# Kernel tuning notes

Hardware: AMD Instinct MI355X
Metric: run time of the kernel (lower is better)

Reference implementation:

```python
import jax, jax.numpy as jnp
import numpy as np

B, S, D, H, E, KW = 2, 2048, 1024, 8, 128, 16  # batch, seq, d_model, heads, head_width, kernel_width


def setup_inputs() -> dict:
    key = jax.random.key(0)
    ks = jax.random.split(key, 10)
    sc = D ** -0.5
    x = jax.random.normal(ks[0], (B, S, D), dtype=jnp.float32)
    Wq = jax.random.normal(ks[1], (H, D, E), dtype=jnp.float32) * sc
    bq = jnp.zeros((H, E), dtype=jnp.float32)
    Wk = jax.random.normal(ks[2], (H, D, E), dtype=jnp.float32) * sc
    bk = jnp.zeros((H, E), dtype=jnp.float32)
    Wv = jax.random.normal(ks[3], (H, D, E), dtype=jnp.float32) * sc
    bv = jnp.zeros((H, E), dtype=jnp.float32)
    Wo = jax.random.normal(ks[4], (H, E, D), dtype=jnp.float32) * ((H * E) ** -0.5)
    bo = jnp.zeros((D,), dtype=jnp.float32)
    dilations = jnp.array([1, 1, 2, 2, 4, 4, 8, 8], dtype=jnp.int32)
    return {"x": x, "Wq": Wq, "bq": bq, "Wk": Wk, "bk": bk,
            "Wv": Wv, "bv": bv, "Wo": Wo, "bo": bo, "dilations": dilations}


def _windows(kh, vh, bkh, bvh, d):
    # kh, vh: [B, S, E] projected keys/values for one head; d: dilation (scalar int)
    s = kh.shape[1]
    # center-justified dilated window: positions i + d*j - d*(KW-1)//2
    pos = jnp.arange(s)[:, None] + d * jnp.arange(KW)[None, :] - (d * (KW - 1)) // 2
    valid = (pos >= 0) & (pos < s)            # [S, KW]
    posc = jnp.clip(pos, 0, s - 1)
    # padded positions hold the zero-embedding, whose projection is just the bias
    kw = jnp.where(valid[None, :, :, None], kh[:, posc, :], bkh)  # [B, S, KW, E]
    vw = jnp.where(valid[None, :, :, None], vh[:, posc, :], bvh)
    return kw, vw


def _lcsa(x, Wq, bq, Wk, bk, Wv, bv, Wo, bo, dilations):
    # per-head independent projections (Core.Linear with parallel shape [heads])
    q = jnp.einsum('bsd,hde->bhse', x, Wq) + bq[None, :, None, :]       # [B,H,S,E]
    k_all = jnp.einsum('bsd,hde->bhse', x, Wk) + bk[None, :, None, :]
    v_all = jnp.einsum('bsd,hde->bhse', x, Wv) + bv[None, :, None, :]
    # gather dilated local windows per head (project-then-gather; padded = bias)
    kw, vw = jax.vmap(_windows, in_axes=(1, 1, 0, 0, 0))(k_all, v_all, bk, bv, dilations)
    # kw, vw: [H, B, S, KW, E]
    logits = jnp.einsum('bhse,hbske->bhsk', q, kw)                       # [B,H,S,KW]
    score = jax.nn.softmax(logits, axis=-1)
    # NOTE: original divides by sqrt(d_head) AFTER softmax*value (faithful quirk)
    attn = jnp.einsum('bhsk,hbske->bhse', score, vw) / jnp.sqrt(jnp.asarray(E, x.dtype))
    out = jnp.einsum('bhse,hed->bsd', attn, Wo) + bo                     # dehead merge
    return out


def reference(x, Wq, bq, Wk, bk, Wv, bv, Wo, bo, dilations):
    return _lcsa(x, Wq, bq, Wk, bk, Wv, bv, Wo, bo, dilations)
```

## Files before the change

kernel.cpp:

```cpp
#include <hip/hip_runtime.h>
#include <stdint.h>

#define Bb 2
#define Ss 2048
#define Dd 1024
#define Hh 8
#define Ee 128
#define KWW 16
#define Mm (Bb*Ss)
#define Kk 1024

typedef unsigned short u16;
typedef __attribute__((ext_vector_type(8))) _Float16 f16x8;
typedef __attribute__((ext_vector_type(4))) float f32x4;

__device__ __forceinline__ u16 f2h(float f) {
  union { _Float16 h; u16 u; } v; v.h = (_Float16)f; return v.u;
}
__device__ __forceinline__ float h2f(u16 u) {
  union { u16 u; _Float16 h; } v; v.u = u; return (float)v.h;
}
__device__ __forceinline__ float h2f_lo(uint32_t w) { return h2f((u16)(w & 0xFFFF)); }
__device__ __forceinline__ float h2f_hi(uint32_t w) { return h2f((u16)(w >> 16)); }

__device__ __forceinline__ void gll16(const void* g, void* l) {
  __builtin_amdgcn_global_load_lds((const __attribute__((address_space(1))) void*)g,
                                   (__attribute__((address_space(3))) void*)l, 16, 0, 0);
}


__global__ __launch_bounds__(256) void cast_f32_f16(const float* __restrict__ in,
                                                    u16* __restrict__ out, int n) {
  int i = (blockIdx.x * 256 + threadIdx.x) * 4;
  if (i < n) {
    float4 f = *(const float4*)(in + i);
    uint64_t pk = (uint64_t)f2h(f.x) | ((uint64_t)f2h(f.y) << 16) |
                  ((uint64_t)f2h(f.z) << 32) | ((uint64_t)f2h(f.w) << 48);
    *(uint64_t*)(out + i) = pk;
  }
}

__global__ __launch_bounds__(256) void transpose_qkv(
    const float* __restrict__ Wq, const float* __restrict__ Wk,
    const float* __restrict__ Wv, u16* __restrict__ wT) {
  __shared__ float tile[32][33];
  const int z = blockIdx.z, h = z & 7;
  const float* W = (z < 8) ? Wq : (z < 16) ? Wk : Wv;
  const float* ib = W + (size_t)h * Dd * Ee;
  u16* ob = wT + (size_t)z * Ee * Kk;
  int r0 = blockIdx.x * 32, c0 = blockIdx.y * 32;
  int tx = threadIdx.x, ty = threadIdx.y;
  #pragma unroll
  for (int kq = 0; kq < 4; kq++)
    tile[ty + 8*kq][tx] = ib[(size_t)(r0 + ty + 8*kq) * Ee + (c0 + tx)];
  __syncthreads();
  #pragma unroll
  for (int kq = 0; kq < 4; kq++)
    ob[(size_t)(c0 + ty + 8*kq) * Dd + (r0 + tx)] = f2h(tile[tx][ty + 8*kq]);
}

__global__ __launch_bounds__(256) void transpose_wo(
    const float* __restrict__ in, u16* __restrict__ out) {
  __shared__ float tile[32][33];
  const int R = Hh * Ee, C = Dd;
  int r0 = blockIdx.x * 32, c0 = blockIdx.y * 32;
  int tx = threadIdx.x, ty = threadIdx.y;
  #pragma unroll
  for (int kq = 0; kq < 4; kq++)
    tile[ty + 8*kq][tx] = in[(size_t)(r0 + ty + 8*kq) * C + (c0 + tx)];
  __syncthreads();
  #pragma unroll
  for (int kq = 0; kq < 4; kq++)
    out[(size_t)(c0 + ty + 8*kq) * R + (r0 + tx)] = f2h(tile[tx][ty + 8*kq]);
}

template<int MT>
__device__ __forceinline__ void gemm_core(
    const u16* __restrict__ A, const u16* __restrict__ Bt,
    u16* As, u16* Bs, f32x4 (&acc)[MT / 32][4]) {
  constexpr int MI = MT / 32;
  const int tid = threadIdx.x;
  const int wave = tid >> 6;
  const int lane = tid & 63;
  const int srow = wave * 16 + (lane >> 2);
  const int skc  = (lane & 3) * 8;
  const size_t go0 = (size_t)srow        * Kk + skc;
  const size_t go1 = (size_t)(srow + 64) * Kk + skc;
  u16* al0 = As + wave * 512;
  u16* al1 = As + 2048 + wave * 512;
  u16* bl0 = Bs + wave * 512;
  u16* bl1 = Bs + 2048 + wave * 512;

  const int wm = (wave >> 1) * (MT / 2);
  const int wn = (wave & 1) * 64;
  const int fr = lane & 15;
  const int fk = (lane >> 4) * 8;

  #pragma unroll
  for (int i = 0; i < MI; i++)
    #pragma unroll
    for (int j = 0; j < 4; j++)
      #pragma unroll
      for (int r = 0; r < 4; r++) acc[i][j][r] = 0.0f;

  for (int kt = 0; kt < Kk; kt += 32) {
    gll16(A + go0 + kt, al0);
    if constexpr (MT == 128) gll16(A + go1 + kt, al1);
    gll16(Bt + go0 + kt, bl0);
    gll16(Bt + go1 + kt, bl1);
    __syncthreads();
    f16x8 ah[MI], bh[4];
    #pragma unroll
    for (int i = 0; i < MI; i++)
      ah[i] = *(const f16x8*)(As + (wm + i * 16 + fr) * 32 + fk);
    #pragma unroll
    for (int j = 0; j < 4; j++)
      bh[j] = *(const f16x8*)(Bs + (wn + j * 16 + fr) * 32 + fk);
    #pragma unroll
    for (int i = 0; i < MI; i++)
      #pragma unroll
      for (int j = 0; j < 4; j++)
        acc[i][j] = __builtin_amdgcn_mfma_f32_16x16x32_f16(ah[i], bh[j], acc[i][j], 0, 0, 0);
    __syncthreads();
  }
}


__global__ __launch_bounds__(256) void gemm_qkv(
    const u16* __restrict__ xh, const u16* __restrict__ wT,
    const float* __restrict__ bq, const float* __restrict__ bk, const float* __restrict__ bv,
    u16* __restrict__ q, u16* __restrict__ k, u16* __restrict__ v) {
  __shared__ u16 As[128 * 32];
  __shared__ u16 Bs[128 * 32];
  const int m0 = blockIdx.x * 128;
  const int z = blockIdx.z;
  const int proj = z >> 3, h = z & 7;
  f32x4 acc[4][4];
  gemm_core<128>(xh + (size_t)m0 * Kk, wT + (size_t)z * (Ee * Kk), As, Bs, acc);

  u16* dst = proj == 0 ? q : (proj == 1 ? k : v);
  const float* bias = proj == 0 ? bq : (proj == 1 ? bk : bv);
  const int wave = threadIdx.x >> 6, lane = threadIdx.x & 63;
  const int wm = (wave >> 1) * 64, wn = (wave & 1) * 64;
  const int cn = lane & 15, rq4 = (lane >> 4) * 4;
  #pragma unroll
  for (int j = 0; j < 4; j++) {
    const int e = wn + j * 16 + cn;
    const float bb = bias[h * Ee + e];
    #pragma unroll
    for (int i = 0; i < 4; i++) {
      #pragma unroll
      for (int r = 0; r < 4; r++) {
        const int m = m0 + wm + i * 16 + rq4 + r;
        const int b = m >> 11, s = m & (Ss - 1);
        dst[(((size_t)(b * Hh + h)) * Ss + s) * Ee + e] = f2h(acc[i][j][r] + bb);
      }
    }
  }
}

__global__ __launch_bounds__(256) void gemm_out(
    const u16* __restrict__ attn, const u16* __restrict__ woT,
    const float* __restrict__ bo, float* __restrict__ out) {
  __shared__ u16 As[64 * 32];
  __shared__ u16 Bs[128 * 32];
  const int m0 = blockIdx.x * 64;
  const int n0 = blockIdx.y * 128;
  f32x4 acc[2][4];
  gemm_core<64>(attn + (size_t)m0 * Kk, woT + (size_t)n0 * Kk, As, Bs, acc);
  const int wave = threadIdx.x >> 6, lane = threadIdx.x & 63;
  const int wm = (wave >> 1) * 32, wn = (wave & 1) * 64;
  const int cn = lane & 15, rq4 = (lane >> 4) * 4;
  #pragma unroll
  for (int j = 0; j < 4; j++) {
    const int n = n0 + wn + j * 16 + cn;
    const float bb = bo[n];
    #pragma unroll
    for (int i = 0; i < 2; i++) {
      #pragma unroll
      for (int r = 0; r < 4; r++) {
        const int m = m0 + wm + i * 16 + rq4 + r;
        out[(size_t)m * Dd + n] = acc[i][j][r] + bb;
      }
    }
  }
}

__global__ __launch_bounds__(256) void attn_kernel(
    const u16* __restrict__ q, const u16* __restrict__ k, const u16* __restrict__ v,
    const float* __restrict__ bk, const float* __restrict__ bv,
    const int* __restrict__ dil, u16* __restrict__ attn) {
  const int nblk = (Bb * Hh * Ss) / 4;
  const int blk = (blockIdx.x & 7) * (nblk / 8) + (blockIdx.x >> 3);
  const int wid = blk * 4 + (threadIdx.x >> 6);
  const int lane = threadIdx.x & 63;
  const int s = wid & (Ss - 1);
  const int bh = wid >> 11;
  const int h = bh & 7, b = bh >> 3;
  const int d = dil[h];
  const size_t base = (size_t)bh * Ss * Ee;
  const u16* kp = k + base;
  const u16* vp = v + base;
  const uint32_t qw = *(const uint32_t*)(q + base + (size_t)s * Ee + 2 * lane);
  const float qx = h2f_lo(qw), qy = h2f_hi(qw);
  const float2 bk2 = ((const float2*)(bk + h * Ee))[lane];
  const float2 bv2 = ((const float2*)(bv + h * Ee))[lane];
  const int off = (d * (KWW - 1)) >> 1;
  const int J = (lane >> 2) & 15;

  float logit[KWW];
  #pragma unroll
  for (int j = 0; j < KWW; j++) {
    const int pos = s + d * j - off;
    if (pos >= 0 && pos < Ss) {
      uint32_t kw = *(const uint32_t*)(kp + (size_t)pos * Ee + 2 * lane);
      logit[j] = qx * h2f_lo(kw) + qy * h2f_hi(kw);
    } else {
      logit[j] = qx * bk2.x + qy * bk2.y;
    }
  }
  float vvx[KWW], vvy[KWW];
  #pragma unroll
  for (int t = 0; t < KWW; t++) {
    const int j = J ^ t;
    const int pos = s + d * j - off;
    const int posc = min(max(pos, 0), Ss - 1);
    uint32_t vw = *(const uint32_t*)(vp + (size_t)posc * Ee + 2 * lane);
    const bool ok = (pos >= 0) && (pos < Ss);
    vvx[t] = ok ? h2f_lo(vw) : bv2.x;
    vvy[t] = ok ? h2f_hi(vw) : bv2.y;
  }

  {
    const bool hi = (lane & 32) != 0;
    #pragma unroll
    for (int j = 0; j < 8; j++) {
      float send = hi ? logit[j] : logit[j + 8];
      float recv = __shfl_xor(send, 32, 64);
      logit[j] = (hi ? logit[j + 8] : logit[j]) + recv;
    }
  }
  {
    const bool hi = (lane & 16) != 0;
    #pragma unroll
    for (int j = 0; j < 4; j++) {
      float send = hi ? logit[j] : logit[j + 4];
      float recv = __shfl_xor(send, 16, 64);
      logit[j] = (hi ? logit[j + 4] : logit[j]) + recv;
    }
  }
  {
    const bool hi = (lane & 8) != 0;
    #pragma unroll
    for (int j = 0; j < 2; j++) {
      float send = hi ? logit[j] : logit[j + 2];
      float recv = __shfl_xor(send, 8, 64);
      logit[j] = (hi ? logit[j + 2] : logit[j]) + recv;
    }
  }
  float own;
  {
    const bool hi = (lane & 4) != 0;
    float send = hi ? logit[0] : logit[1];
    float recv = __shfl_xor(send, 4, 64);
    own = (hi ? logit[1] : logit[0]) + recv;
  }
  own += __shfl_xor(own, 2, 64);
  own += __shfl_xor(own, 1, 64);

  float mx = own;
  mx = fmaxf(mx, __shfl_xor(mx, 4, 64));
  mx = fmaxf(mx, __shfl_xor(mx, 8, 64));
  mx = fmaxf(mx, __shfl_xor(mx, 16, 64));
  mx = fmaxf(mx, __shfl_xor(mx, 32, 64));
  float w = __expf(own - mx);
  float sum = w;
  sum += __shfl_xor(sum, 4, 64);
  sum += __shfl_xor(sum, 8, 64);
  sum += __shfl_xor(sum, 16, 64);
  sum += __shfl_xor(sum, 32, 64);
  w *= 1.0f / (sum * 11.313708498984760f);

  float g[KWW];
  g[0] = w;
  g[1] = __shfl_xor(g[0], 4, 64);
  #pragma unroll
  for (int t = 0; t < 2; t++) g[2 + t] = __shfl_xor(g[t], 8, 64);
  #pragma unroll
  for (int t = 0; t < 4; t++) g[4 + t] = __shfl_xor(g[t], 16, 64);
  #pragma unroll
  for (int t = 0; t < 8; t++) g[8 + t] = __shfl_xor(g[t], 32, 64);

  float ax = 0.f, ay = 0.f;
  #pragma unroll
  for (int t = 0; t < KWW; t++) { ax += g[t] * vvx[t]; ay += g[t] * vvy[t]; }

  u16* op = attn + ((size_t)(b * Ss + s)) * (Hh * Ee) + h * Ee + 2 * lane;
  *(uint32_t*)op = (uint32_t)f2h(ax) | ((uint32_t)f2h(ay) << 16);
}

extern "C" void kernel_launch(void* const* d_in, const int* in_sizes, int n_in,
                              void* d_out, int out_size, void* d_ws, size_t ws_size,
                              hipStream_t stream) {
  (void)in_sizes; (void)n_in; (void)out_size; (void)ws_size;
  const float* x  = (const float*)d_in[0];
  const float* Wq = (const float*)d_in[1];
  const float* bq = (const float*)d_in[2];
  const float* Wk = (const float*)d_in[3];
  const float* bk = (const float*)d_in[4];
  const float* Wv = (const float*)d_in[5];
  const float* bv = (const float*)d_in[6];
  const float* Wo = (const float*)d_in[7];
  const float* bo = (const float*)d_in[8];
  const int* dil  = (const int*)d_in[9];
  float* out = (float*)d_out;

  char* ws = (char*)d_ws;
  u16* xh  = (u16*)ws;  ws += (size_t)Mm * Kk * 2;
  u16* wT  = (u16*)ws;  ws += (size_t)24 * Ee * Kk * 2;
  u16* woT = (u16*)ws;  ws += (size_t)Kk * Dd * 2;
  u16* q = (u16*)ws; ws += (size_t)Bb * Hh * Ss * Ee * 2;
  u16* k = (u16*)ws; ws += (size_t)Bb * Hh * Ss * Ee * 2;
  u16* v = (u16*)ws; ws += (size_t)Bb * Hh * Ss * Ee * 2;
  u16* attn = xh;

  cast_f32_f16<<<(Mm * Kk) / 1024, 256, 0, stream>>>(x, xh, Mm * Kk);
  dim3 tb(32, 8);
  transpose_qkv<<<dim3(Dd / 32, Ee / 32, 24), tb, 0, stream>>>(Wq, Wk, Wv, wT);
  transpose_wo<<<dim3((Hh * Ee) / 32, Dd / 32, 1), tb, 0, stream>>>(Wo, woT);

  gemm_qkv<<<dim3(Mm / 128, 1, 24), 256, 0, stream>>>(xh, wT, bq, bk, bv, q, k, v);
  attn_kernel<<<(Bb * Hh * Ss) / 4, 256, 0, stream>>>(q, k, v, bk, bv, dil, attn);
  gemm_out<<<dim3(Mm / 64, Dd / 128), 256, 0, stream>>>(attn, woT, bo, out);
}
```

Baseline: 179.9 us.

## Merge prep kernels and double GEMM K-tile with XOR-swizzled LDS layout

Folds the x cast and the two weight-transpose kernels into a single launch that dispatches on block index, removing two kernel launches. The shared GEMM core now loads a K-tile of 64 instead of 32 per sync, halving the barrier count and doubling the MFMAs per stage. It also XOR-swizzles the 16-byte chunks in LDS to avoid bank conflicts on fragment reads. LDS per block doubles, which could lower occupancy.

Result: slower. 187.2 us (+4.1%).

```diff
diff --git a/kernel.cpp b/kernel.cpp
--- a/kernel.cpp
+++ b/kernel.cpp
@@ -28,50 +28,50 @@
                                    (__attribute__((address_space(3))) void*)l, 16, 0, 0);
 }
 
-
-__global__ __launch_bounds__(256) void cast_f32_f16(const float* __restrict__ in,
-                                                    u16* __restrict__ out, int n) {
-  int i = (blockIdx.x * 256 + threadIdx.x) * 4;
-  if (i < n) {
-    float4 f = *(const float4*)(in + i);
+__global__ __launch_bounds__(256) void prep(
+    const float* __restrict__ x, const float* __restrict__ Wq,
+    const float* __restrict__ Wk, const float* __restrict__ Wv,
+    const float* __restrict__ Wo,
+    u16* __restrict__ xh, u16* __restrict__ wT, u16* __restrict__ woT) {
+  const int bid = blockIdx.x;
+  const int tid = threadIdx.x;
+  if (bid < 4096) {
+    int i = (bid * 256 + tid) * 4;
+    float4 f = *(const float4*)(x + i);
     uint64_t pk = (uint64_t)f2h(f.x) | ((uint64_t)f2h(f.y) << 16) |
                   ((uint64_t)f2h(f.z) << 32) | ((uint64_t)f2h(f.w) << 48);
-    *(uint64_t*)(out + i) = pk;
-  }
-}
-
-__global__ __launch_bounds__(256) void transpose_qkv(
-    const float* __restrict__ Wq, const float* __restrict__ Wk,
-    const float* __restrict__ Wv, u16* __restrict__ wT) {
+    *(uint64_t*)(xh + i) = pk;
+    return;
+  }
   __shared__ float tile[32][33];
-  const int z = blockIdx.z, h = z & 7;
-  const float* W = (z < 8) ? Wq : (z < 16) ? Wk : Wv;
-  const float* ib = W + (size_t)h * Dd * Ee;
-  u16* ob = wT + (size_t)z * Ee * Kk;
-  int r0 = blockIdx.x * 32, c0 = blockIdx.y * 32;
-  int tx = threadIdx.x, ty = threadIdx.y;
-  #pragma unroll
-  for (int kq = 0; kq < 4; kq++)
-    tile[ty + 8*kq][tx] = ib[(size_t)(r0 + ty + 8*kq) * Ee + (c0 + tx)];
-  __syncthreads();
-  #pragma unroll
-  for (int kq = 0; kq < 4; kq++)
-    ob[(size_t)(c0 + ty + 8*kq) * Dd + (r0 + tx)] = f2h(tile[tx][ty + 8*kq]);
-}
-
-__global__ __launch_bounds__(256) void transpose_wo(
-    const float* __restrict__ in, u16* __restrict__ out) {
-  __shared__ float tile[32][33];
-  const int R = Hh * Ee, C = Dd;
-  int r0 = blockIdx.x * 32, c0 = blockIdx.y * 32;
-  int tx = threadIdx.x, ty = threadIdx.y;
-  #pragma unroll
-  for (int kq = 0; kq < 4; kq++)
-    tile[ty + 8*kq][tx] = in[(size_t)(r0 + ty + 8*kq) * C + (c0 + tx)];
-  __syncthreads();
-  #pragma unroll
-  for (int kq = 0; kq < 4; kq++)
-    out[(size_t)(c0 + ty + 8*kq) * R + (r0 + tx)] = f2h(tile[tx][ty + 8*kq]);
+  const int tx = tid & 31, ty = tid >> 5;
+  if (bid < 4096 + 3072) {
+    const int idx = bid - 4096;
+    const int z = idx >> 7, rem = idx & 127;
+    const int h = z & 7;
+    const float* W = (z < 8) ? Wq : (z < 16) ? Wk : Wv;
+    const float* ib = W + (size_t)h * Dd * Ee;
+    u16* ob = wT + (size_t)z * Ee * Kk;
+    const int r0 = (rem & 31) * 32, c0 = (rem >> 5) * 32;
+    #pragma unroll
+    for (int kq = 0; kq < 4; kq++)
+      tile[ty + 8*kq][tx] = ib[(size_t)(r0 + ty + 8*kq) * Ee + (c0 + tx)];
+    __syncthreads();
+    #pragma unroll
+    for (int kq = 0; kq < 4; kq++)
+      ob[(size_t)(c0 + ty + 8*kq) * Dd + (r0 + tx)] = f2h(tile[tx][ty + 8*kq]);
+  } else {
+    const int idx = bid - (4096 + 3072);
+    const int r0 = (idx & 31) * 32, c0 = (idx >> 5) * 32;
+    const int R = Hh * Ee, C = Dd;
+    #pragma unroll
+    for (int kq = 0; kq < 4; kq++)
+      tile[ty + 8*kq][tx] = Wo[(size_t)(r0 + ty + 8*kq) * C + (c0 + tx)];
+    __syncthreads();
+    #pragma unroll
+    for (int kq = 0; kq < 4; kq++)
+      woT[(size_t)(c0 + ty + 8*kq) * R + (r0 + tx)] = f2h(tile[tx][ty + 8*kq]);
+  }
 }
 
 template<int MT>
@@ -82,19 +82,13 @@
   const int tid = threadIdx.x;
   const int wave = tid >> 6;
   const int lane = tid & 63;
-  const int srow = wave * 16 + (lane >> 2);
-  const int skc  = (lane & 3) * 8;
-  const size_t go0 = (size_t)srow        * Kk + skc;
-  const size_t go1 = (size_t)(srow + 64) * Kk + skc;
-  u16* al0 = As + wave * 512;
-  u16* al1 = As + 2048 + wave * 512;
-  u16* bl0 = Bs + wave * 512;
-  u16* bl1 = Bs + 2048 + wave * 512;
+  const size_t lnoff = (size_t)(lane >> 3) * Kk + (size_t)(((lane & 7) ^ (lane >> 3)) * 8);
 
   const int wm = (wave >> 1) * (MT / 2);
   const int wn = (wave & 1) * 64;
   const int fr = lane & 15;
-  const int fk = (lane >> 4) * 8;
+  const int q  = lane >> 4;
+  const int sw = fr & 7;
 
   #pragma unroll
   for (int i = 0; i < MI; i++)
@@ -103,24 +97,30 @@
       #pragma unroll
       for (int r = 0; r < 4; r++) acc[i][j][r] = 0.0f;
 
-  for (int kt = 0; kt < Kk; kt += 32) {
-    gll16(A + go0 + kt, al0);
-    if constexpr (MT == 128) gll16(A + go1 + kt, al1);
-    gll16(Bt + go0 + kt, bl0);
-    gll16(Bt + go1 + kt, bl1);
+  for (int kt = 0; kt < Kk; kt += 64) {
+    #pragma unroll
+    for (int c = 0; c < MI * 2; c++)
+      gll16(A + lnoff + (size_t)((c * 4 + wave) * 8) * Kk + kt, As + (c * 4 + wave) * 512);
+    #pragma unroll
+    for (int c = 0; c < 4; c++)
+      gll16(Bt + lnoff + (size_t)((c * 4 + wave) * 8) * Kk + kt, Bs + (c * 4 + wave) * 512);
     __syncthreads();
-    f16x8 ah[MI], bh[4];
-    #pragma unroll
-    for (int i = 0; i < MI; i++)
-      ah[i] = *(const f16x8*)(As + (wm + i * 16 + fr) * 32 + fk);
-    #pragma unroll
-    for (int j = 0; j < 4; j++)
-      bh[j] = *(const f16x8*)(Bs + (wn + j * 16 + fr) * 32 + fk);
-    #pragma unroll
-    for (int i = 0; i < MI; i++)
+    #pragma unroll
+    for (int ks = 0; ks < 2; ks++) {
+      const int col = ((ks << 2) | q) ^ sw;
+      f16x8 ah[MI], bh[4];
+      #pragma unroll
+      for (int i = 0; i < MI; i++)
+        ah[i] = *(const f16x8*)(As + (wm + i * 16 + fr) * 64 + col * 8);
       #pragma unroll
       for (int j = 0; j < 4; j++)
-        acc[i][j] = __builtin_amdgcn_mfma_f32_16x16x32_f16(ah[i], bh[j], acc[i][j], 0, 0, 0);
+        bh[j] = *(const f16x8*)(Bs + (wn + j * 16 + fr) * 64 + col * 8);
+      #pragma unroll
+      for (int i = 0; i < MI; i++)
+        #pragma unroll
+        for (int j = 0; j < 4; j++)
+          acc[i][j] = __builtin_amdgcn_mfma_f32_16x16x32_f16(ah[i], bh[j], acc[i][j], 0, 0, 0);
+    }
     __syncthreads();
   }
 }
@@ -130,8 +130,8 @@
     const u16* __restrict__ xh, const u16* __restrict__ wT,
     const float* __restrict__ bq, const float* __restrict__ bk, const float* __restrict__ bv,
     u16* __restrict__ q, u16* __restrict__ k, u16* __restrict__ v) {
-  __shared__ u16 As[128 * 32];
-  __shared__ u16 Bs[128 * 32];
+  __shared__ u16 As[128 * 64];
+  __shared__ u16 Bs[128 * 64];
   const int m0 = blockIdx.x * 128;
   const int z = blockIdx.z;
   const int proj = z >> 3, h = z & 7;
@@ -162,8 +162,8 @@
 __global__ __launch_bounds__(256) void gemm_out(
     const u16* __restrict__ attn, const u16* __restrict__ woT,
     const float* __restrict__ bo, float* __restrict__ out) {
-  __shared__ u16 As[64 * 32];
-  __shared__ u16 Bs[128 * 32];
+  __shared__ u16 As[64 * 64];
+  __shared__ u16 Bs[128 * 64];
   const int m0 = blockIdx.x * 64;
   const int n0 = blockIdx.y * 128;
   f32x4 acc[2][4];
@@ -324,11 +324,7 @@
   u16* v = (u16*)ws; ws += (size_t)Bb * Hh * Ss * Ee * 2;
   u16* attn = xh;
 
-  cast_f32_f16<<<(Mm * Kk) / 1024, 256, 0, stream>>>(x, xh, Mm * Kk);
-  dim3 tb(32, 8);
-  transpose_qkv<<<dim3(Dd / 32, Ee / 32, 24), tb, 0, stream>>>(Wq, Wk, Wv, wT);
-  transpose_wo<<<dim3((Hh * Ee) / 32, Dd / 32, 1), tb, 0, stream>>>(Wo, woT);
-
+  prep<<<8192, 256, 0, stream>>>(x, Wq, Wk, Wv, Wo, xh, wT, woT);
   gemm_qkv<<<dim3(Mm / 128, 1, 24), 256, 0, stream>>>(xh, wT, bq, bk, bv, q, k, v);
   attn_kernel<<<(Bb * Hh * Ss) / 4, 256, 0, stream>>>(q, k, v, bk, bv, dil, attn);
   gemm_out<<<dim3(Mm / 64, Dd / 128), 256, 0, stream>>>(attn, woT, bo, out);
```
